# Performance work log

Measured on AMD Instinct MI355X. Metric: run time of the kernel, lower is better.

The kernel has to match this reference:

```python
import jax, jax.numpy as jnp
import numpy as np

K = 16          # nsample / knn k
GROUPS = 4      # GroupNorm groups
EPS = 1e-5


def setup_inputs() -> dict:
    key = jax.random.key(0)
    ks = jax.random.split(key, 10)
    B, N = 8, 2048
    x = jax.random.normal(ks[0], (B, 3, N), jnp.float32)
    f = x  # at first call features == coordinates
    w = lambda i, shape: jax.random.normal(ks[i], shape, jnp.float32) * 0.05
    return dict(
        x=x, f=f,
        # input_trans: Conv1d(3 -> 64)
        W_it=w(1, (64, 3)), b_it=jnp.zeros((64,), jnp.float32),
        # layer1: Conv2d(128 -> 128, bias=False) + GroupNorm(4, 128)
        W1=w(2, (128, 128)), gn_g=jnp.ones((128,), jnp.float32), gn_b=jnp.zeros((128,), jnp.float32),
        # mlp1: Conv2d(128->256), Conv2d(256->512)
        Wa=w(3, (256, 128)), ba=jnp.zeros((256,), jnp.float32),
        Wb=w(4, (512, 256)), bb=jnp.zeros((512,), jnp.float32),
        # mlp2: Conv1d(640->256), Conv1d(256->128)
        Wc=w(5, (256, 640)), bc=jnp.zeros((256,), jnp.float32),
        Wd=w(6, (128, 256)), bd=jnp.zeros((128,), jnp.float32),
        # mlp3: Conv1d(128->256), Conv1d(256->512)
        We=w(7, (256, 128)), be=jnp.zeros((256,), jnp.float32),
        Wf=w(8, (512, 256)), bf=jnp.zeros((512,), jnp.float32),
    )


def _knn_idx(x):
    # x: (B, 3, N) -> idx: (B, N, K) indices of K nearest neighbors (self-knn)
    coor = jnp.transpose(x, (0, 2, 1))                       # (B, N, 3)
    sq = jnp.sum(coor * coor, axis=-1)                        # (B, N)
    d = sq[:, :, None] + sq[:, None, :] - 2.0 * jnp.einsum('bnc,bmc->bnm', coor, coor)
    _, idx = jax.lax.top_k(-d, K)                             # smallest distances
    return idx


def _group_norm(y, gamma, beta):
    # y: (B, N, K, C); torch GroupNorm normalizes over (C/g, N, K) per (b, group)
    B, N, Kk, C = y.shape
    yg = y.reshape(B, N, Kk, GROUPS, C // GROUPS)
    mu = jnp.mean(yg, axis=(1, 2, 4), keepdims=True)
    var = jnp.var(yg, axis=(1, 2, 4), keepdims=True)
    yg = (yg - mu) * jax.lax.rsqrt(var + EPS)
    return yg.reshape(B, N, Kk, C) * gamma + beta


def reference(x, f, W_it, b_it, W1, gn_g, gn_b, Wa, ba, Wb, bb, Wc, bc, Wd, bd, We, be, Wf, bf):
    B, _, N = x.shape
    idx = _knn_idx(x)                                          # (B, N, K)

    # input_trans: 1x1 conv over channels, channels-last layout (B, N, C)
    h = jnp.einsum('bcn,oc->bno', f, W_it) + b_it              # (B, N, 64)

    # graph feature: gather neighbors, build [nb - h, h]
    nb = jax.vmap(lambda hb, ib: hb[ib])(h, idx)               # (B, N, K, 64)
    hq = h[:, :, None, :]                                       # (B, N, 1, 64)
    feat = jnp.concatenate([nb - hq, jnp.broadcast_to(hq, nb.shape)], axis=-1)  # (B, N, K, 128)

    # layer1: conv1x1 (no bias) + GroupNorm + LeakyReLU(0.2)
    y = jnp.einsum('bnkc,oc->bnko', feat, W1)                  # (B, N, K, 128)
    y = jax.nn.leaky_relu(_group_norm(y, gn_g, gn_b), 0.2)

    local_base = jnp.max(y, axis=2)                             # (B, N, 128)

    # mlp1 over edges, then max over K and global max over N
    g = jax.nn.relu(jnp.einsum('bnkc,oc->bnko', y, Wa) + ba)    # (B, N, K, 256)
    g = jax.nn.relu(jnp.einsum('bnkc,oc->bnko', g, Wb) + bb)    # (B, N, K, 512)
    gfeat = jnp.max(g, axis=2)                                  # (B, N, 512)
    gmax = jnp.max(gfeat, axis=1, keepdims=True)                # (B, 1, 512)

    cat = jnp.concatenate([local_base, jnp.broadcast_to(gmax, (B, N, 512))], axis=-1)  # (B, N, 640)

    lf = jax.nn.relu(jnp.einsum('bnc,oc->bno', cat, Wc) + bc)   # (B, N, 256)
    lf = jax.nn.relu(jnp.einsum('bnc,oc->bno', lf, Wd) + bd)    # (B, N, 128)

    gl = jax.nn.relu(jnp.einsum('bnc,oc->bno', lf, We) + be)    # (B, N, 256)
    gl = jax.nn.relu(jnp.einsum('bnc,oc->bno', gl, Wf) + bf)    # (B, N, 512)
    gl = jnp.max(gl, axis=1, keepdims=True)                     # (B, 1, 512)

    global_feat = jnp.transpose(gl, (0, 2, 1))                  # (B, 512, 1)
    local_feat = jnp.transpose(lf, (0, 2, 1))                   # (B, 128, N)
    return (global_feat, local_feat)
```

## Files before the change

### kernel.cpp

```cpp
#include <hip/hip_runtime.h>
#include <hip/hip_bf16.h>

#define BATCH 8
#define NPTS 2048
#define KNNK 16
#define CH 64
#define CF 128
#define CA 256
#define CB 512
#define CCAT 640
#define CC 256
#define CD 128
#define CE 256
#define CG 512
#define NGRP 4
#define EPSF 1e-5f
#define GF_OFF (BATCH*CG)
#define P 8
#define MROWS (P*KNNK)
#define TM 64

typedef __attribute__((ext_vector_type(8))) short short8v;
typedef __attribute__((ext_vector_type(4))) float f32x4;

__device__ inline short f2bf(float f) {
  __hip_bfloat16 h = __float2bfloat16(f);
  return *reinterpret_cast<short*>(&h);
}

#define LIDX(r, c, ROW) ((r)*(ROW) + ((c) ^ (((r)&7)<<3)))

__device__ inline void pack_dev(const float* __restrict__ W, short* __restrict__ Wp,
                                int O, int C, int ld, int tid) {
  int KS = C >> 5;
  int total = (O >> 4) * KS * 64;
  if (tid >= total) return;
  int l = tid & 63;
  int fs = tid >> 6;
  int nt = fs / KS, ks = fs - nt * KS;
  int o = nt * 16 + (l & 15);
  int c = ks * 32 + (l >> 4) * 8;
  const float* src = W + (size_t)o * ld + c;
  short8v v;
#pragma unroll
  for (int j = 0; j < 8; ++j) v[j] = f2bf(src[j]);
  *(short8v*)&Wp[(size_t)tid * 8] = v;
}

__global__ __launch_bounds__(256)
void k_prep(const float* __restrict__ f, const float* __restrict__ Wit,
            const float* __restrict__ bit, float* __restrict__ h,
            const float* __restrict__ W1, short* __restrict__ W1p,
            const float* __restrict__ Wa, short* __restrict__ Wap,
            const float* __restrict__ Wb, short* __restrict__ Wbp,
            const float* __restrict__ Wc, short* __restrict__ WcLp,
            const float* __restrict__ Wd, short* __restrict__ Wdp,
            const float* __restrict__ We, short* __restrict__ Wep,
            const float* __restrict__ Wf, short* __restrict__ Wfp) {
  int blk = blockIdx.x;
  if (blk < 4096) {
    int t = blk * 256 + threadIdx.x;
    int o = t & (CH - 1);
    int bn = t >> 6;
    int n = bn & (NPTS - 1);
    int b = bn >> 11;
    float f0 = f[(b*3 + 0)*NPTS + n];
    float f1 = f[(b*3 + 1)*NPTS + n];
    float f2 = f[(b*3 + 2)*NPTS + n];
    h[t] = f0*Wit[o*3+0] + f1*Wit[o*3+1] + f2*Wit[o*3+2] + bit[o];
  } else if (blk < 4104) pack_dev(W1, W1p, CF, CF, CF, (blk-4096)*256 + threadIdx.x);
  else if (blk < 4120) pack_dev(Wa, Wap, CA, CF, CF, (blk-4104)*256 + threadIdx.x);
  else if (blk < 4184) pack_dev(Wb, Wbp, CB, CA, CA, (blk-4120)*256 + threadIdx.x);
  else if (blk < 4200) pack_dev(Wc, WcLp, CC, CF, CCAT, (blk-4184)*256 + threadIdx.x);
  else if (blk < 4216) pack_dev(Wd, Wdp, CD, CC, CC, (blk-4200)*256 + threadIdx.x);
  else if (blk < 4232) pack_dev(We, Wep, CE, CD, CD, (blk-4216)*256 + threadIdx.x);
  else                 pack_dev(Wf, Wfp, CG, CE, CE, (blk-4232)*256 + threadIdx.x);
}

__global__ __launch_bounds__(512)
void k_knn(const float* __restrict__ x, int* __restrict__ idxout) {
  __shared__ float xs0[2112], xs1[2112], xs2[2112], sqs[2112];
  int blk = blockIdx.x;
  int b = blk >> 8;
  int n0 = (blk & 255) * 8;
  int t = threadIdx.x;
  for (int i = t; i < NPTS; i += 512) {
    float x0 = x[(b*3 + 0)*NPTS + i];
    float x1 = x[(b*3 + 1)*NPTS + i];
    float x2 = x[(b*3 + 2)*NPTS + i];
    int a = (i >> 5)*33 + (i & 31);
    xs0[a] = x0; xs1[a] = x1; xs2[a] = x2;
    sqs[a] = __fadd_rn(__fadd_rn(__fmul_rn(x0,x0), __fmul_rn(x1,x1)), __fmul_rn(x2,x2));
  }
  __syncthreads();
  int lane = t & 63, wv = t >> 6;
  int q = n0 + wv;
  int qa = (q >> 5)*33 + (q & 31);
  float qx = xs0[qa], qy = xs1[qa], qz = xs2[qa];
  float sqq = sqs[qa];
  float d[32];
  int base = lane * 32;
#pragma unroll
  for (int jj = 0; jj < 32; ++jj) {
    int a = lane*33 + jj;
    float mx = xs0[a], my = xs1[a], mz = xs2[a];
    float dot = __fadd_rn(__fadd_rn(__fmul_rn(qx,mx), __fmul_rn(qy,my)), __fmul_rn(qz,mz));
    d[jj] = __fsub_rn(__fadd_rn(sqq, sqs[a]), __fadd_rn(dot, dot));
  }
  const float FINF = __builtin_inff();
  float sv0 = d[0]; int si0 = base;
#pragma unroll
  for (int jj = 1; jj < 16; ++jj)
    if (d[jj] < sv0) { sv0 = d[jj]; si0 = base + jj; }
  float sv1 = d[16]; int si1 = base + 16;
#pragma unroll
  for (int jj = 17; jj < 32; ++jj)
    if (d[jj] < sv1) { sv1 = d[jj]; si1 = base + jj; }
  int gsel = 0;
#pragma unroll
  for (int r = 0; r < KNNK; ++r) {
    float v = sv0; int i = si0;
    if (sv1 < v || (sv1 == v && si1 < i)) { v = sv1; i = si1; }
#pragma unroll
    for (int off = 32; off > 0; off >>= 1) {
      float v2 = __shfl_xor(v, off);
      int   i2 = __shfl_xor(i, off);
      if (v2 < v || (v2 == v && i2 < i)) { v = v2; i = i2; }
    }
    if (lane == r) gsel = i;
    int rem = ((i >> 5) == lane) ? (i & 31) : 64;
    if (rem < 16) {
      float nv = FINF; int ni = 0x7fffffff;
#pragma unroll
      for (int jj = 0; jj < 16; ++jj) {
        float dv = (jj == rem) ? FINF : d[jj];
        d[jj] = dv;
        if (dv < nv) { nv = dv; ni = base + jj; }
      }
      sv0 = nv; si0 = ni;
    } else if (rem < 32) {
      float nv = FINF; int ni = 0x7fffffff;
#pragma unroll
      for (int jj = 16; jj < 32; ++jj) {
        float dv = (jj == rem) ? FINF : d[jj];
        d[jj] = dv;
        if (dv < nv) { nv = dv; ni = base + jj; }
      }
      sv1 = nv; si1 = ni;
    }
  }
  if (lane < KNNK) idxout[(size_t)(b*NPTS + q)*KNNK + lane] = gsel;
}

__device__ inline void stage_feat(short* featS, const float* __restrict__ h,
                                  const int* __restrict__ idx, int b, int n0, int t) {
  int r = t >> 1, cb = (t & 1) * 32;
  int p = r >> 4, kk = r & 15;
  int nbi = idx[(size_t)(b*NPTS + n0 + p)*KNNK + kk];
  const float* hq = h + (size_t)(b*NPTS + n0 + p)*CH;
  const float* hn = h + (size_t)(b*NPTS + nbi)*CH;
#pragma unroll
  for (int j = 0; j < 32; j += 8) {
    float4 q0 = *(const float4*)(hq + cb + j);
    float4 q1 = *(const float4*)(hq + cb + j + 4);
    float4 a0 = *(const float4*)(hn + cb + j);
    float4 a1 = *(const float4*)(hn + cb + j + 4);
    short8v dv, qv;
    dv[0]=f2bf(a0.x-q0.x); dv[1]=f2bf(a0.y-q0.y); dv[2]=f2bf(a0.z-q0.z); dv[3]=f2bf(a0.w-q0.w);
    dv[4]=f2bf(a1.x-q1.x); dv[5]=f2bf(a1.y-q1.y); dv[6]=f2bf(a1.z-q1.z); dv[7]=f2bf(a1.w-q1.w);
    qv[0]=f2bf(q0.x); qv[1]=f2bf(q0.y); qv[2]=f2bf(q0.z); qv[3]=f2bf(q0.w);
    qv[4]=f2bf(q1.x); qv[5]=f2bf(q1.y); qv[6]=f2bf(q1.z); qv[7]=f2bf(q1.w);
    *(short8v*)&featS[LIDX(r, cb + j, CF)] = dv;
    *(short8v*)&featS[LIDX(r, 64 + cb + j, CF)] = qv;
  }
}

__global__ __launch_bounds__(256, 2)
void k_stats(const float* __restrict__ h, const int* __restrict__ idx,
             const short* __restrict__ W1p, float* __restrict__ partials) {
  __shared__ short featS[MROWS*CF];
  int blk = blockIdx.x;
  int b = blk >> 8;
  int n0 = (blk & 255) * P;
  int t = threadIdx.x;
  stage_feat(featS, h, idx, b, n0, t);
  __syncthreads();
  int lane = t & 63, wv = t >> 6;
  int r16 = lane & 15, g8 = (lane >> 4) * 8;
  float s = 0.f, ss = 0.f;
#pragma unroll
  for (int mh = 0; mh < 2; ++mh) {
    short8v af[4][4];
#pragma unroll
    for (int mm = 0; mm < 4; ++mm)
#pragma unroll
      for (int ks = 0; ks < 4; ++ks)
        af[mm][ks] = *(const short8v*)&featS[LIDX((mh*4+mm)*16 + r16, ks*32 + g8, CF)];
#pragma unroll
    for (int n = 0; n < 2; ++n) {
      int nt = 2*wv + n;
      short8v bfr[4];
#pragma unroll
      for (int ks = 0; ks < 4; ++ks)
        bfr[ks] = *(const short8v*)&W1p[(size_t)((nt*4 + ks)*64 + lane)*8];
#pragma unroll
      for (int mm = 0; mm < 4; ++mm) {
        f32x4 acc = {0.f, 0.f, 0.f, 0.f};
#pragma unroll
        for (int ks = 0; ks < 4; ++ks)
          acc = __builtin_amdgcn_mfma_f32_16x16x32_bf16(af[mm][ks], bfr[ks], acc, 0, 0, 0);
#pragma unroll
        for (int i = 0; i < 4; ++i) { s += acc[i]; ss += acc[i]*acc[i]; }
      }
    }
  }
#pragma unroll
  for (int off = 32; off > 0; off >>= 1) {
    s += __shfl_xor(s, off);
    ss += __shfl_xor(ss, off);
  }
  if (lane == 0) {
    partials[(size_t)(blk*NGRP + wv)*2 + 0] = s;
    partials[(size_t)(blk*NGRP + wv)*2 + 1] = ss;
  }
}

__global__ void k_reduce(const float* __restrict__ partials, float* __restrict__ stats) {
  int b = blockIdx.x >> 2, g = blockIdx.x & 3;
  int t = threadIdx.x;
  float s  = partials[(size_t)((b*256 + t)*NGRP + g)*2 + 0];
  float ss = partials[(size_t)((b*256 + t)*NGRP + g)*2 + 1];
  __shared__ float rs[256], rss[256];
  rs[t] = s; rss[t] = ss;
  __syncthreads();
  for (int st = 128; st > 0; st >>= 1) {
    if (t < st) { rs[t] += rs[t+st]; rss[t] += rss[t+st]; }
    __syncthreads();
  }
  if (t == 0) {
    const float cnt = (float)((size_t)NPTS * KNNK * 32);
    float mu = rs[0] / cnt;
    float var = rss[0] / cnt - mu*mu;
    stats[(b*NGRP+g)*2+0] = mu;
    stats[(b*NGRP+g)*2+1] = rsqrtf(var + EPSF);
  }
}

__global__ __launch_bounds__(256, 2)
void k_main(const float* __restrict__ h, const int* __restrict__ idx,
            const short* __restrict__ W1p, const float* __restrict__ gng,
            const float* __restrict__ gnb, const float* __restrict__ stats,
            const short* __restrict__ Wap, const float* __restrict__ ba,
            const short* __restrict__ Wbp, const float* __restrict__ bb,
            float* __restrict__ lbase, unsigned* __restrict__ gmaxU) {
  __shared__ short lds[MROWS*CA];
  short* featS = lds;
  short* ynS   = lds + MROWS*CF;
  short* g1S   = lds;
  int blk = blockIdx.x;
  int b = blk >> 8;
  int n0 = (blk & 255) * P;
  int t = threadIdx.x;
  stage_feat(featS, h, idx, b, n0, t);
  __syncthreads();
  int lane = t & 63, wv = t >> 6;
  int r16 = lane & 15, g8 = (lane >> 4) * 8;
  int rowg = (lane >> 4) * 4;
  {
    short8v af[8][4];
#pragma unroll
    for (int m = 0; m < 8; ++m)
#pragma unroll
      for (int ks = 0; ks < 4; ++ks)
        af[m][ks] = *(const short8v*)&featS[LIDX(m*16 + r16, ks*32 + g8, CF)];
    float mu  = stats[(b*NGRP + wv)*2 + 0];
    float rsg = stats[(b*NGRP + wv)*2 + 1];
#pragma unroll
    for (int n = 0; n < 2; ++n) {
      int nt = 2*wv + n;
      int o = nt*16 + r16;
      short8v bfr[4];
#pragma unroll
      for (int ks = 0; ks < 4; ++ks)
        bfr[ks] = *(const short8v*)&W1p[(size_t)((nt*4 + ks)*64 + lane)*8];
      float ga = gng[o], bev = gnb[o];
#pragma unroll
      for (int m = 0; m < 8; ++m) {
        f32x4 acc = {0.f, 0.f, 0.f, 0.f};
#pragma unroll
        for (int ks = 0; ks < 4; ++ks)
          acc = __builtin_amdgcn_mfma_f32_16x16x32_bf16(af[m][ks], bfr[ks], acc, 0, 0, 0);
        float vmax = -3.0e38f;
#pragma unroll
        for (int i = 0; i < 4; ++i) {
          float v = (acc[i] - mu) * rsg * ga + bev;
          v = (v >= 0.f) ? v : 0.2f*v;
          vmax = fmaxf(vmax, v);
          ynS[LIDX(m*16 + rowg + i, o, CF)] = f2bf(v);
        }
        vmax = fmaxf(vmax, __shfl_xor(vmax, 16));
        vmax = fmaxf(vmax, __shfl_xor(vmax, 32));
        if (lane < 16) lbase[(size_t)(b*NPTS + n0 + m)*CF + o] = vmax;
      }
    }
  }
  __syncthreads();
  {
    short8v yf[8][4];
#pragma unroll
    for (int m = 0; m < 8; ++m)
#pragma unroll
      for (int ks = 0; ks < 4; ++ks)
        yf[m][ks] = *(const short8v*)&ynS[LIDX(m*16 + r16, ks*32 + g8, CF)];
    __syncthreads();
#pragma unroll
    for (int nn = 0; nn < 4; ++nn) {
      int nt = wv*4 + nn;
      int o = nt*16 + r16;
      short8v bfr[4];
#pragma unroll
      for (int ks = 0; ks < 4; ++ks)
        bfr[ks] = *(const short8v*)&Wap[(size_t)((nt*4 + ks)*64 + lane)*8];
      float bav = ba[o];
#pragma unroll
      for (int m = 0; m < 8; ++m) {
        f32x4 acc = {0.f, 0.f, 0.f, 0.f};
#pragma unroll
        for (int ks = 0; ks < 4; ++ks)
          acc = __builtin_amdgcn_mfma_f32_16x16x32_bf16(yf[m][ks], bfr[ks], acc, 0, 0, 0);
#pragma unroll
        for (int i = 0; i < 4; ++i) {
          float v = fmaxf(acc[i] + bav, 0.f);
          g1S[LIDX(m*16 + rowg + i, o, CA)] = f2bf(v);
        }
      }
    }
  }
  __syncthreads();
#pragma unroll
  for (int half = 0; half < 2; ++half) {
    f32x4 acc[4][8];
#pragma unroll
    for (int nn = 0; nn < 4; ++nn)
#pragma unroll
      for (int m = 0; m < 8; ++m) acc[nn][m] = (f32x4){0.f, 0.f, 0.f, 0.f};
#pragma unroll
    for (int ks = 0; ks < 8; ++ks) {
      short8v gfk[8];
#pragma unroll
      for (int m = 0; m < 8; ++m)
        gfk[m] = *(const short8v*)&g1S[LIDX(m*16 + r16, ks*32 + g8, CA)];
#pragma unroll
      for (int nn = 0; nn < 4; ++nn) {
        int nt = wv*8 + half*4 + nn;
        short8v bfr = *(const short8v*)&Wbp[(size_t)((nt*8 + ks)*64 + lane)*8];
#pragma unroll
        for (int m = 0; m < 8; ++m)
          acc[nn][m] = __builtin_amdgcn_mfma_f32_16x16x32_bf16(gfk[m], bfr, acc[nn][m], 0, 0, 0);
      }
    }
#pragma unroll
    for (int nn = 0; nn < 4; ++nn) {
      int nt = wv*8 + half*4 + nn;
      float b0 = bb[nt*16 + r16];
      float am = 0.f;
#pragma unroll
      for (int m = 0; m < 8; ++m)
#pragma unroll
        for (int i = 0; i < 4; ++i) am = fmaxf(am, acc[nn][m][i] + b0);
      am = fmaxf(am, __shfl_xor(am, 16));
      am = fmaxf(am, __shfl_xor(am, 32));
      if (lane < 16) atomicMax(&gmaxU[b*CG + nt*16 + lane], __float_as_uint(am));
    }
  }
}

__global__ __launch_bounds__(256)
void k_gbias(const unsigned* __restrict__ gmaxU, const float* __restrict__ Wc,
             const float* __restrict__ bc, float* __restrict__ bceff) {
  __shared__ float gs[CB];
  int blk = blockIdx.x;
  int b = blk >> 5, og = blk & 31;
  int t = threadIdx.x;
  int lane = t & 63, wv = t >> 6;
  for (int i = t; i < CB; i += 256) gs[i] = __uint_as_float(gmaxU[b*CG + i]);
  __syncthreads();
#pragma unroll
  for (int j = 0; j < 2; ++j) {
    int o = og*8 + wv*2 + j;
    float acc = 0.f;
#pragma unroll
    for (int c8 = 0; c8 < 8; ++c8) {
      int c = lane + c8*64;
      acc += gs[c] * Wc[(size_t)o*CCAT + CF + c];
    }
#pragma unroll
    for (int off = 32; off > 0; off >>= 1) acc += __shfl_xor(acc, off);
    if (lane == 0) bceff[b*CC + o] = bc[o] + acc;
  }
}

__global__ __launch_bounds__(512)
void k_tail(const float* __restrict__ lbase, const float* __restrict__ bceff,
            const short* __restrict__ WcLp,
            const short* __restrict__ Wdp, const float* __restrict__ bd,
            const short* __restrict__ Wep, const float* __restrict__ be,
            const short* __restrict__ Wfp, const float* __restrict__ bf,
            float* __restrict__ out, unsigned* __restrict__ glmaxU) {
  __shared__ short aS0[TM*CF];
  __shared__ short aS1[TM*CA];
  int blk = blockIdx.x;
  int b = blk >> 5;
  int n0 = (blk & 31) * TM;
  int t = threadIdx.x;
  int lane = t & 63, wv = t >> 6;
  {
    int r = t & 63, cs = (t >> 6) * 16;
    const float* src = lbase + (size_t)(b*NPTS + n0 + r)*CF + cs;
#pragma unroll
    for (int j = 0; j < 16; j += 8) {
      float4 v0 = *(const float4*)(src + j);
      float4 v1 = *(const float4*)(src + j + 4);
      short8v pv;
      pv[0]=f2bf(v0.x); pv[1]=f2bf(v0.y); pv[2]=f2bf(v0.z); pv[3]=f2bf(v0.w);
      pv[4]=f2bf(v1.x); pv[5]=f2bf(v1.y); pv[6]=f2bf(v1.z); pv[7]=f2bf(v1.w);
      *(short8v*)&aS0[LIDX(r, cs + j, CF)] = pv;
    }
  }
  __syncthreads();
  int r16 = lane & 15, g8 = (lane >> 4) * 8;
  int rowg = (lane >> 4) * 4;
  {
    short8v af[4][4];
#pragma unroll
    for (int mt = 0; mt < 4; ++mt)
#pragma unroll
      for (int ks = 0; ks < 4; ++ks)
        af[mt][ks] = *(const short8v*)&aS0[LIDX(mt*16 + r16, ks*32 + g8, CF)];
#pragma unroll
    for (int nn = 0; nn < 2; ++nn) {
      int nt = wv*2 + nn;
      int o = nt*16 + r16;
      short8v bfr[4];
#pragma unroll
      for (int ks = 0; ks < 4; ++ks)
        bfr[ks] = *(const short8v*)&WcLp[(size_t)((nt*4 + ks)*64 + lane)*8];
      float bce = bceff[b*CC + o];
#pragma unroll
      for (int mt = 0; mt < 4; ++mt) {
        f32x4 acc = {0.f, 0.f, 0.f, 0.f};
#pragma unroll
        for (int ks = 0; ks < 4; ++ks)
          acc = __builtin_amdgcn_mfma_f32_16x16x32_bf16(af[mt][ks], bfr[ks], acc, 0, 0, 0);
#pragma unroll
        for (int i = 0; i < 4; ++i)
          aS1[LIDX(mt*16 + rowg + i, o, CA)] = f2bf(fmaxf(acc[i] + bce, 0.f));
      }
    }
  }
  __syncthreads();
  {
    short8v af[4][8];
#pragma unroll
    for (int mt = 0; mt < 4; ++mt)
#pragma unroll
      for (int ks = 0; ks < 8; ++ks)
        af[mt][ks] = *(const short8v*)&aS1[LIDX(mt*16 + r16, ks*32 + g8, CA)];
    {
      int nt = wv;
      int o = nt*16 + r16;
      short8v bfr[8];
#pragma unroll
      for (int ks = 0; ks < 8; ++ks)
        bfr[ks] = *(const short8v*)&Wdp[(size_t)((nt*8 + ks)*64 + lane)*8];
      float bdv = bd[o];
#pragma unroll
      for (int mt = 0; mt < 4; ++mt) {
        f32x4 acc = {0.f, 0.f, 0.f, 0.f};
#pragma unroll
        for (int ks = 0; ks < 8; ++ks)
          acc = __builtin_amdgcn_mfma_f32_16x16x32_bf16(af[mt][ks], bfr[ks], acc, 0, 0, 0);
#pragma unroll
        for (int i = 0; i < 4; ++i) {
          float v = fmaxf(acc[i] + bdv, 0.f);
          aS0[LIDX(mt*16 + rowg + i, o, CF)] = f2bf(v);
          out[GF_OFF + ((size_t)(b*CD + o))*NPTS + n0 + mt*16 + rowg + i] = v;
        }
      }
    }
  }
  __syncthreads();
  {
    short8v af[4][4];
#pragma unroll
    for (int mt = 0; mt < 4; ++mt)
#pragma unroll
      for (int ks = 0; ks < 4; ++ks)
        af[mt][ks] = *(const short8v*)&aS0[LIDX(mt*16 + r16, ks*32 + g8, CF)];
#pragma unroll
    for (int nn = 0; nn < 2; ++nn) {
      int nt = wv*2 + nn;
      int o = nt*16 + r16;
      short8v bfr[4];
#pragma unroll
      for (int ks = 0; ks < 4; ++ks)
        bfr[ks] = *(const short8v*)&Wep[(size_t)((nt*4 + ks)*64 + lane)*8];
      float bev = be[o];
#pragma unroll
      for (int mt = 0; mt < 4; ++mt) {
        f32x4 acc = {0.f, 0.f, 0.f, 0.f};
#pragma unroll
        for (int ks = 0; ks < 4; ++ks)
          acc = __builtin_amdgcn_mfma_f32_16x16x32_bf16(af[mt][ks], bfr[ks], acc, 0, 0, 0);
#pragma unroll
        for (int i = 0; i < 4; ++i)
          aS1[LIDX(mt*16 + rowg + i, o, CA)] = f2bf(fmaxf(acc[i] + bev, 0.f));
      }
    }
  }
  __syncthreads();
  {
    short8v af[4][8];
#pragma unroll
    for (int mt = 0; mt < 4; ++mt)
#pragma unroll
      for (int ks = 0; ks < 8; ++ks)
        af[mt][ks] = *(const short8v*)&aS1[LIDX(mt*16 + r16, ks*32 + g8, CA)];
#pragma unroll
    for (int nn = 0; nn < 4; ++nn) {
      int nt = wv*4 + nn;
      short8v bfr[8];
#pragma unroll
      for (int ks = 0; ks < 8; ++ks)
        bfr[ks] = *(const short8v*)&Wfp[(size_t)((nt*8 + ks)*64 + lane)*8];
      float bfv = bf[nt*16 + r16];
      float am = 0.f;
#pragma unroll
      for (int mt = 0; mt < 4; ++mt) {
        f32x4 acc = {0.f, 0.f, 0.f, 0.f};
#pragma unroll
        for (int ks = 0; ks < 8; ++ks)
          acc = __builtin_amdgcn_mfma_f32_16x16x32_bf16(af[mt][ks], bfr[ks], acc, 0, 0, 0);
#pragma unroll
        for (int i = 0; i < 4; ++i) am = fmaxf(am, acc[i] + bfv);
      }
      am = fmaxf(am, __shfl_xor(am, 16));
      am = fmaxf(am, __shfl_xor(am, 32));
      if (lane < 16) atomicMax(&glmaxU[b*CG + nt*16 + lane], __float_as_uint(am));
    }
  }
}

__global__ void k_final(const unsigned* __restrict__ glmaxU, float* __restrict__ out) {
  int i = blockIdx.x*256 + threadIdx.x;
  if (i < BATCH*CG) out[i] = __uint_as_float(glmaxU[i]);
}

extern "C" void kernel_launch(void* const* d_in, const int* in_sizes, int n_in,
                              void* d_out, int out_size, void* d_ws, size_t ws_size,
                              hipStream_t stream) {
  const float* x   = (const float*)d_in[0];
  const float* f   = (const float*)d_in[1];
  const float* Wit = (const float*)d_in[2];
  const float* bit = (const float*)d_in[3];
  const float* W1  = (const float*)d_in[4];
  const float* gng = (const float*)d_in[5];
  const float* gnb = (const float*)d_in[6];
  const float* Wa  = (const float*)d_in[7];
  const float* ba  = (const float*)d_in[8];
  const float* Wb  = (const float*)d_in[9];
  const float* bb  = (const float*)d_in[10];
  const float* Wc  = (const float*)d_in[11];
  const float* bc  = (const float*)d_in[12];
  const float* Wd  = (const float*)d_in[13];
  const float* bd  = (const float*)d_in[14];
  const float* We  = (const float*)d_in[15];
  const float* be  = (const float*)d_in[16];
  const float* Wf  = (const float*)d_in[17];
  const float* bf  = (const float*)d_in[18];
  float* out = (float*)d_out;

  char* w = (char*)d_ws;
  size_t off = 0;
  auto alloc = [&](size_t bytes) {
    void* p = w + off; off += (bytes + 255) & ~(size_t)255; return p;
  };
  float* h        = (float*)alloc((size_t)BATCH*NPTS*CH*4);
  int*   idx      = (int*)  alloc((size_t)BATCH*NPTS*KNNK*4);
  short* W1p      = (short*)alloc((size_t)CF*CF*2);
  short* Wap      = (short*)alloc((size_t)CA*CF*2);
  short* Wbp      = (short*)alloc((size_t)CB*CA*2);
  short* WcLp     = (short*)alloc((size_t)CC*CF*2);
  short* Wdp      = (short*)alloc((size_t)CD*CC*2);
  short* Wep      = (short*)alloc((size_t)CE*CD*2);
  short* Wfp      = (short*)alloc((size_t)CG*CE*2);
  float* bceff    = (float*)alloc((size_t)BATCH*CC*4);
  float* partials = (float*)alloc((size_t)(BATCH*NPTS/P)*NGRP*2*4);
  float* stats    = (float*)alloc((size_t)BATCH*NGRP*2*4);
  float* lbase    = (float*)alloc((size_t)BATCH*NPTS*CF*4);
  unsigned* gmaxU  = (unsigned*)alloc((size_t)BATCH*CG*4);
  unsigned* glmaxU = (unsigned*)alloc((size_t)BATCH*CG*4);

  hipMemsetAsync(gmaxU, 0, (size_t)BATCH*CG*4, stream);
  hipMemsetAsync(glmaxU, 0, (size_t)BATCH*CG*4, stream);

  k_prep<<<4296, 256, 0, stream>>>(f, Wit, bit, h, W1, W1p, Wa, Wap, Wb, Wbp,
                                   Wc, WcLp, Wd, Wdp, We, Wep, Wf, Wfp);
  k_knn<<<BATCH*NPTS/8, 512, 0, stream>>>(x, idx);
  k_stats<<<BATCH*NPTS/P, 256, 0, stream>>>(h, idx, W1p, partials);
  k_reduce<<<BATCH*NGRP, 256, 0, stream>>>(partials, stats);
  k_main<<<BATCH*NPTS/P, 256, 0, stream>>>(h, idx, W1p, gng, gnb, stats,
                                           Wap, ba, Wbp, bb, lbase, gmaxU);
  k_gbias<<<BATCH*32, 256, 0, stream>>>(gmaxU, Wc, bc, bceff);
  k_tail<<<BATCH*NPTS/TM, 512, 0, stream>>>(lbase, bceff, WcLp, Wdp, bd,
                                            Wep, be, Wfp, bf, out, glmaxU);
  k_final<<<(BATCH*CG+255)/256, 256, 0, stream>>>(glmaxU, out);
}
```

Before: 255.2 us.

## Fold reduce/final kernels into last-block epilogues and widen main kernel to 512 threads

The separate k_reduce and k_final launches are removed. k_stats and k_tail now take an atomic ticket counter, and the last block to finish does the group-stat reduction or the output copy after a threadfence. k_main moves to 512 threads (8 waves), each wave owning half the output tiles, with feature staging split across twice as many threads. Layer-a is split into two row halves to cut register pressure. The aim is to save two launches and raise occupancy or latency hiding in the main kernel, at the cost of an extra memset and the serial tail work done by the last block.

```diff
diff --git a/kernel.cpp b/kernel.cpp
--- a/kernel.cpp
+++ b/kernel.cpp
@@ -177,8 +177,10 @@
 
 __global__ __launch_bounds__(256, 2)
 void k_stats(const float* __restrict__ h, const int* __restrict__ idx,
-             const short* __restrict__ W1p, float* __restrict__ partials) {
+             const short* __restrict__ W1p, float* __restrict__ partials,
+             float* __restrict__ stats, unsigned* __restrict__ tick) {
   __shared__ short featS[MROWS*CF];
+  __shared__ int lastFlag;
   int blk = blockIdx.x;
   int b = blk >> 8;
   int n0 = (blk & 255) * P;
@@ -223,30 +225,42 @@
     partials[(size_t)(blk*NGRP + wv)*2 + 0] = s;
     partials[(size_t)(blk*NGRP + wv)*2 + 1] = ss;
   }
-}
-
-__global__ void k_reduce(const float* __restrict__ partials, float* __restrict__ stats) {
-  int b = blockIdx.x >> 2, g = blockIdx.x & 3;
-  int t = threadIdx.x;
-  float s  = partials[(size_t)((b*256 + t)*NGRP + g)*2 + 0];
-  float ss = partials[(size_t)((b*256 + t)*NGRP + g)*2 + 1];
-  __shared__ float rs[256], rss[256];
-  rs[t] = s; rss[t] = ss;
-  __syncthreads();
-  for (int st = 128; st > 0; st >>= 1) {
-    if (t < st) { rs[t] += rs[t+st]; rss[t] += rss[t+st]; }
-    __syncthreads();
-  }
+  __syncthreads();
   if (t == 0) {
-    const float cnt = (float)((size_t)NPTS * KNNK * 32);
-    float mu = rs[0] / cnt;
-    float var = rss[0] / cnt - mu*mu;
-    stats[(b*NGRP+g)*2+0] = mu;
-    stats[(b*NGRP+g)*2+1] = rsqrtf(var + EPSF);
-  }
-}
-
-__global__ __launch_bounds__(256, 2)
+    __threadfence();
+    lastFlag = (atomicAdd(tick, 1u) == (unsigned)(gridDim.x - 1)) ? 1 : 0;
+  }
+  __syncthreads();
+  if (lastFlag) {
+    __threadfence();
+#pragma unroll
+    for (int j = 0; j < 8; ++j) {
+      int p = wv*8 + j;
+      int bb_ = p >> 2, g = p & 3;
+      float rs = 0.f, rss = 0.f;
+#pragma unroll
+      for (int c = 0; c < 4; ++c) {
+        int tile = bb_*256 + lane + c*64;
+        rs  += partials[((size_t)tile*NGRP + g)*2 + 0];
+        rss += partials[((size_t)tile*NGRP + g)*2 + 1];
+      }
+#pragma unroll
+      for (int off = 32; off > 0; off >>= 1) {
+        rs += __shfl_xor(rs, off);
+        rss += __shfl_xor(rss, off);
+      }
+      if (lane == 0) {
+        const float cnt = (float)((size_t)NPTS * KNNK * 32);
+        float mu = rs / cnt;
+        float var = rss / cnt - mu*mu;
+        stats[(bb_*NGRP+g)*2+0] = mu;
+        stats[(bb_*NGRP+g)*2+1] = rsqrtf(var + EPSF);
+      }
+    }
+  }
+}
+
+__global__ __launch_bounds__(512)
 void k_main(const float* __restrict__ h, const int* __restrict__ idx,
             const short* __restrict__ W1p, const float* __restrict__ gng,
             const float* __restrict__ gnb, const float* __restrict__ stats,
@@ -261,35 +275,66 @@
   int b = blk >> 8;
   int n0 = (blk & 255) * P;
   int t = threadIdx.x;
-  stage_feat(featS, h, idx, b, n0, t);
+  {
+    int r = t >> 2, q4 = (t & 3) * 32;
+    int p = r >> 4, kk = r & 15;
+    const float* hq = h + (size_t)(b*NPTS + n0 + p)*CH;
+    if (q4 < 64) {
+      int nbi = idx[(size_t)(b*NPTS + n0 + p)*KNNK + kk];
+      const float* hn = h + (size_t)(b*NPTS + nbi)*CH;
+#pragma unroll
+      for (int j = 0; j < 32; j += 8) {
+        float4 q0 = *(const float4*)(hq + q4 + j);
+        float4 q1 = *(const float4*)(hq + q4 + j + 4);
+        float4 a0 = *(const float4*)(hn + q4 + j);
+        float4 a1 = *(const float4*)(hn + q4 + j + 4);
+        short8v dv;
+        dv[0]=f2bf(a0.x-q0.x); dv[1]=f2bf(a0.y-q0.y); dv[2]=f2bf(a0.z-q0.z); dv[3]=f2bf(a0.w-q0.w);
+        dv[4]=f2bf(a1.x-q1.x); dv[5]=f2bf(a1.y-q1.y); dv[6]=f2bf(a1.z-q1.z); dv[7]=f2bf(a1.w-q1.w);
+        *(short8v*)&featS[LIDX(r, q4 + j, CF)] = dv;
+      }
+    } else {
+      int cb = q4 - 64;
+#pragma unroll
+      for (int j = 0; j < 32; j += 8) {
+        float4 q0 = *(const float4*)(hq + cb + j);
+        float4 q1 = *(const float4*)(hq + cb + j + 4);
+        short8v qv;
+        qv[0]=f2bf(q0.x); qv[1]=f2bf(q0.y); qv[2]=f2bf(q0.z); qv[3]=f2bf(q0.w);
+        qv[4]=f2bf(q1.x); qv[5]=f2bf(q1.y); qv[6]=f2bf(q1.z); qv[7]=f2bf(q1.w);
+        *(short8v*)&featS[LIDX(r, q4 + j, CF)] = qv;
+      }
+    }
+  }
   __syncthreads();
   int lane = t & 63, wv = t >> 6;
   int r16 = lane & 15, g8 = (lane >> 4) * 8;
   int rowg = (lane >> 4) * 4;
   {
-    short8v af[8][4];
-#pragma unroll
-    for (int m = 0; m < 8; ++m)
-#pragma unroll
-      for (int ks = 0; ks < 4; ++ks)
-        af[m][ks] = *(const short8v*)&featS[LIDX(m*16 + r16, ks*32 + g8, CF)];
-    float mu  = stats[(b*NGRP + wv)*2 + 0];
-    float rsg = stats[(b*NGRP + wv)*2 + 1];
-#pragma unroll
-    for (int n = 0; n < 2; ++n) {
-      int nt = 2*wv + n;
-      int o = nt*16 + r16;
-      short8v bfr[4];
-#pragma unroll
-      for (int ks = 0; ks < 4; ++ks)
-        bfr[ks] = *(const short8v*)&W1p[(size_t)((nt*4 + ks)*64 + lane)*8];
-      float ga = gng[o], bev = gnb[o];
-#pragma unroll
-      for (int m = 0; m < 8; ++m) {
+    int nt = wv;
+    int o = nt*16 + r16;
+    short8v bfr[4];
+#pragma unroll
+    for (int ks = 0; ks < 4; ++ks)
+      bfr[ks] = *(const short8v*)&W1p[(size_t)((nt*4 + ks)*64 + lane)*8];
+    float mu  = stats[(b*NGRP + (wv>>1))*2 + 0];
+    float rsg = stats[(b*NGRP + (wv>>1))*2 + 1];
+    float ga = gng[o], bev = gnb[o];
+#pragma unroll
+    for (int mh = 0; mh < 2; ++mh) {
+      short8v af[4][4];
+#pragma unroll
+      for (int mm = 0; mm < 4; ++mm)
+#pragma unroll
+        for (int ks = 0; ks < 4; ++ks)
+          af[mm][ks] = *(const short8v*)&featS[LIDX((mh*4+mm)*16 + r16, ks*32 + g8, CF)];
+#pragma unroll
+      for (int mm = 0; mm < 4; ++mm) {
+        int m = mh*4 + mm;
         f32x4 acc = {0.f, 0.f, 0.f, 0.f};
 #pragma unroll
         for (int ks = 0; ks < 4; ++ks)
-          acc = __builtin_amdgcn_mfma_f32_16x16x32_bf16(af[m][ks], bfr[ks], acc, 0, 0, 0);
+          acc = __builtin_amdgcn_mfma_f32_16x16x32_bf16(af[mm][ks], bfr[ks], acc, 0, 0, 0);
         float vmax = -3.0e38f;
 #pragma unroll
         for (int i = 0; i < 4; ++i) {
@@ -306,16 +351,15 @@
   }
   __syncthreads();
   {
-    short8v yf[8][4];
-#pragma unroll
-    for (int m = 0; m < 8; ++m)
-#pragma unroll
-      for (int ks = 0; ks < 4; ++ks)
-        yf[m][ks] = *(const short8v*)&ynS[LIDX(m*16 + r16, ks*32 + g8, CF)];
-    __syncthreads();
-#pragma unroll
-    for (int nn = 0; nn < 4; ++nn) {
-      int nt = wv*4 + nn;
+    short8v yf[4][4];
+#pragma unroll
+    for (int mm = 0; mm < 4; ++mm)
+#pragma unroll
+      for (int ks = 0; ks < 4; ++ks)
+        yf[mm][ks] = *(const short8v*)&ynS[LIDX(mm*16 + r16, ks*32 + g8, CF)];
+#pragma unroll
+    for (int nn = 0; nn < 2; ++nn) {
+      int nt = wv*2 + nn;
       int o = nt*16 + r16;
       short8v bfr[4];
 #pragma unroll
@@ -323,25 +367,54 @@
         bfr[ks] = *(const short8v*)&Wap[(size_t)((nt*4 + ks)*64 + lane)*8];
       float bav = ba[o];
 #pragma unroll
-      for (int m = 0; m < 8; ++m) {
+      for (int mm = 0; mm < 4; ++mm) {
         f32x4 acc = {0.f, 0.f, 0.f, 0.f};
 #pragma unroll
         for (int ks = 0; ks < 4; ++ks)
-          acc = __builtin_amdgcn_mfma_f32_16x16x32_bf16(yf[m][ks], bfr[ks], acc, 0, 0, 0);
+          acc = __builtin_amdgcn_mfma_f32_16x16x32_bf16(yf[mm][ks], bfr[ks], acc, 0, 0, 0);
 #pragma unroll
         for (int i = 0; i < 4; ++i) {
           float v = fmaxf(acc[i] + bav, 0.f);
-          g1S[LIDX(m*16 + rowg + i, o, CA)] = f2bf(v);
+          g1S[LIDX(mm*16 + rowg + i, o, CA)] = f2bf(v);
         }
       }
     }
+    short8v yf1[4][4];
+#pragma unroll
+    for (int mm = 0; mm < 4; ++mm)
+#pragma unroll
+      for (int ks = 0; ks < 4; ++ks)
+        yf1[mm][ks] = *(const short8v*)&ynS[LIDX((4+mm)*16 + r16, ks*32 + g8, CF)];
+    __syncthreads();
+#pragma unroll
+    for (int nn = 0; nn < 2; ++nn) {
+      int nt = wv*2 + nn;
+      int o = nt*16 + r16;
+      short8v bfr[4];
+#pragma unroll
+      for (int ks = 0; ks < 4; ++ks)
+        bfr[ks] = *(const short8v*)&Wap[(size_t)((nt*4 + ks)*64 + lane)*8];
+      float bav = ba[o];
+#pragma unroll
+      for (int mm = 0; mm < 4; ++mm) {
+        f32x4 acc = {0.f, 0.f, 0.f, 0.f};
+#pragma unroll
+        for (int ks = 0; ks < 4; ++ks)
+          acc = __builtin_amdgcn_mfma_f32_16x16x32_bf16(yf1[mm][ks], bfr[ks], acc, 0, 0, 0);
+#pragma unroll
+        for (int i = 0; i < 4; ++i) {
+          float v = fmaxf(acc[i] + bav, 0.f);
+          g1S[LIDX((4+mm)*16 + rowg + i, o, CA)] = f2bf(v);
+        }
+      }
+    }
   }
   __syncthreads();
 #pragma unroll
   for (int half = 0; half < 2; ++half) {
-    f32x4 acc[4][8];
-#pragma unroll
-    for (int nn = 0; nn < 4; ++nn)
+    f32x4 acc[2][8];
+#pragma unroll
+    for (int nn = 0; nn < 2; ++nn)
 #pragma unroll
       for (int m = 0; m < 8; ++m) acc[nn][m] = (f32x4){0.f, 0.f, 0.f, 0.f};
 #pragma unroll
@@ -351,8 +424,8 @@
       for (int m = 0; m < 8; ++m)
         gfk[m] = *(const short8v*)&g1S[LIDX(m*16 + r16, ks*32 + g8, CA)];
 #pragma unroll
-      for (int nn = 0; nn < 4; ++nn) {
-        int nt = wv*8 + half*4 + nn;
+      for (int nn = 0; nn < 2; ++nn) {
+        int nt = wv*4 + half*2 + nn;
         short8v bfr = *(const short8v*)&Wbp[(size_t)((nt*8 + ks)*64 + lane)*8];
 #pragma unroll
         for (int m = 0; m < 8; ++m)
@@ -360,8 +433,8 @@
       }
     }
 #pragma unroll
-    for (int nn = 0; nn < 4; ++nn) {
-      int nt = wv*8 + half*4 + nn;
+    for (int nn = 0; nn < 2; ++nn) {
+      int nt = wv*4 + half*2 + nn;
       float b0 = bb[nt*16 + r16];
       float am = 0.f;
 #pragma unroll
@@ -406,9 +479,11 @@
             const short* __restrict__ Wdp, const float* __restrict__ bd,
             const short* __restrict__ Wep, const float* __restrict__ be,
             const short* __restrict__ Wfp, const float* __restrict__ bf,
-            float* __restrict__ out, unsigned* __restrict__ glmaxU) {
+            float* __restrict__ out, unsigned* __restrict__ glmaxU,
+            unsigned* __restrict__ tick) {
   __shared__ short aS0[TM*CF];
   __shared__ short aS1[TM*CA];
+  __shared__ int lastFlag;
   int blk = blockIdx.x;
   int b = blk >> 5;
   int n0 = (blk & 31) * TM;
@@ -549,11 +624,20 @@
       if (lane < 16) atomicMax(&glmaxU[b*CG + nt*16 + lane], __float_as_uint(am));
     }
   }
-}
-
-__global__ void k_final(const unsigned* __restrict__ glmaxU, float* __restrict__ out) {
-  int i = blockIdx.x*256 + threadIdx.x;
-  if (i < BATCH*CG) out[i] = __uint_as_float(glmaxU[i]);
+  __syncthreads();
+  if (t == 0) {
+    __threadfence();
+    lastFlag = (atomicAdd(tick, 1u) == (unsigned)(gridDim.x - 1)) ? 1 : 0;
+  }
+  __syncthreads();
+  if (lastFlag) {
+    __threadfence();
+#pragma unroll
+    for (int j = 0; j < 8; ++j) {
+      int i = t + j*512;
+      out[i] = __uint_as_float(glmaxU[i]);
+    }
+  }
 }
 
 extern "C" void kernel_launch(void* const* d_in, const int* in_sizes, int n_in,
@@ -600,19 +684,19 @@
   float* lbase    = (float*)alloc((size_t)BATCH*NPTS*CF*4);
   unsigned* gmaxU  = (unsigned*)alloc((size_t)BATCH*CG*4);
   unsigned* glmaxU = (unsigned*)alloc((size_t)BATCH*CG*4);
+  unsigned* ticks  = (unsigned*)alloc(2*4);
 
   hipMemsetAsync(gmaxU, 0, (size_t)BATCH*CG*4, stream);
   hipMemsetAsync(glmaxU, 0, (size_t)BATCH*CG*4, stream);
+  hipMemsetAsync(ticks, 0, 2*4, stream);
 
   k_prep<<<4296, 256, 0, stream>>>(f, Wit, bit, h, W1, W1p, Wa, Wap, Wb, Wbp,
                                    Wc, WcLp, Wd, Wdp, We, Wep, Wf, Wfp);
   k_knn<<<BATCH*NPTS/8, 512, 0, stream>>>(x, idx);
-  k_stats<<<BATCH*NPTS/P, 256, 0, stream>>>(h, idx, W1p, partials);
-  k_reduce<<<BATCH*NGRP, 256, 0, stream>>>(partials, stats);
-  k_main<<<BATCH*NPTS/P, 256, 0, stream>>>(h, idx, W1p, gng, gnb, stats,
+  k_stats<<<BATCH*NPTS/P, 256, 0, stream>>>(h, idx, W1p, partials, stats, &ticks[0]);
+  k_main<<<BATCH*NPTS/P, 512, 0, stream>>>(h, idx, W1p, gng, gnb, stats,
                                            Wap, ba, Wbp, bb, lbase, gmaxU);
   k_gbias<<<BATCH*32, 256, 0, stream>>>(gmaxU, Wc, bc, bceff);
   k_tail<<<BATCH*NPTS/TM, 512, 0, stream>>>(lbase, bceff, WcLp, Wdp, bd,
-                                            Wep, be, Wfp, bf, out, glmaxU);
-  k_final<<<(BATCH*CG+255)/256, 256, 0, stream>>>(glmaxU, out);
-}
+                                            Wep, be, Wfp, bf, out, glmaxU, &ticks[1]);
+}
```

Measured after the change: 325.4 us. 1.28x slower.
